# Kernel optimization log

Hardware: AMD Instinct MI355X
Metric: run time of the kernel (lower is better)

## Reference

```python
import jax, jax.numpy as jnp
import numpy as np

NUM_GRAPHS = 512
BN_EPS = 1e-5

def _lin(k, fin, fout):
    kw, kb = jax.random.split(k)
    s = 1.0 / np.sqrt(fin)
    return (jax.random.uniform(kw, (fin, fout), jnp.float32, -s, s),
            jax.random.uniform(kb, (fout,), jnp.float32, -s, s))

def setup_inputs() -> dict:
    key = jax.random.key(0)
    ks = jax.random.split(key, 16)
    N, E, F, C, H, O = 50000, 800000, 128, 256, 512, 768
    x = jax.random.normal(ks[0], (N, F), jnp.float32)
    edge_index = jax.random.randint(ks[1], (2, E), 0, N, jnp.int64)
    batch = jnp.sort(jax.random.randint(ks[2], (N,), 0, NUM_GRAPHS, jnp.int64))
    d = {"x": x, "edge_index": edge_index, "batch": batch}
    d["w1a"], d["b1a"] = _lin(ks[3], F, C)
    d["g1"], d["be1"] = jnp.ones((C,), jnp.float32), jnp.zeros((C,), jnp.float32)
    d["w1b"], d["b1b"] = _lin(ks[4], C, C)
    d["w2a"], d["b2a"] = _lin(ks[5], C, C)
    d["g2"], d["be2"] = jnp.ones((C,), jnp.float32), jnp.zeros((C,), jnp.float32)
    d["w2b"], d["b2b"] = _lin(ks[6], C, C)
    d["w3a"], d["b3a"] = _lin(ks[7], C, C)
    d["g3"], d["be3"] = jnp.ones((C,), jnp.float32), jnp.zeros((C,), jnp.float32)
    d["w3b"], d["b3b"] = _lin(ks[8], C, C)
    d["wh1"], d["bh1"] = _lin(ks[9], C, H)
    d["wh2"], d["bh2"] = _lin(ks[10], H, O)
    return d

def _bn(z, g, b):
    mu = jnp.mean(z, axis=0)
    var = jnp.mean((z - mu) ** 2, axis=0)  # biased var, torch BN training mode
    return (z - mu) * jax.lax.rsqrt(var + BN_EPS) * g + b

def _gin(x, edge_index, wa, ba, g, be, wb, bb, tanh_out):
    src, dst = edge_index[0], edge_index[1]
    agg = jax.ops.segment_sum(x[src], dst, num_segments=x.shape[0])
    h = x + agg  # eps = 0
    z = jax.nn.relu(_bn(h @ wa + ba, g, be))
    z = z @ wb + bb
    return jnp.tanh(z) if tanh_out else z

def reference(x, edge_index, batch,
              w1a, b1a, g1, be1, w1b, b1b,
              w2a, b2a, g2, be2, w2b, b2b,
              w3a, b3a, g3, be3, w3b, b3b,
              wh1, bh1, wh2, bh2):
    h = jax.nn.relu(_gin(x, edge_index, w1a, b1a, g1, be1, w1b, b1b, False))
    h = jax.nn.relu(_gin(h, edge_index, w2a, b2a, g2, be2, w2b, b2b, True))
    h = _gin(h, edge_index, w3a, b3a, g3, be3, w3b, b3b, True)
    # global mean pool over graphs
    sums = jax.ops.segment_sum(h, batch, num_segments=NUM_GRAPHS)
    cnt = jax.ops.segment_sum(jnp.ones((h.shape[0],), h.dtype), batch, num_segments=NUM_GRAPHS)
    pooled = sums / jnp.maximum(cnt, 1.0)[:, None]
    z = jax.nn.relu(pooled @ wh1 + bh1)
    return z @ wh2 + bh2
```

## Files before the change

### kernel.cpp

```cpp
#include <hip/hip_runtime.h>


typedef __attribute__((ext_vector_type(8))) short short8;
typedef __attribute__((ext_vector_type(4))) float f32x4;
typedef __attribute__((ext_vector_type(4))) unsigned short us4;
typedef __attribute__((ext_vector_type(8))) unsigned short us8;

__device__ __forceinline__ unsigned short f2bf(float f) {
  unsigned int b = __float_as_uint(f);
  unsigned int r = 0x7FFFu + ((b >> 16) & 1u);
  return (unsigned short)((b + r) >> 16);
}
__device__ __forceinline__ float bf2f(unsigned short u) {
  return __uint_as_float(((unsigned int)u) << 16);
}

__device__ __forceinline__ int swv(int row) {
  return (row & 3) ^ ((row >> 2) & 3);
}

typedef const __attribute__((address_space(1))) unsigned int* gas1;
typedef __attribute__((address_space(3))) unsigned int* las3;
__device__ __forceinline__ void gload16(const void* g, void* l) {
  __builtin_amdgcn_global_load_lds((gas1)g, (las3)l, 16, 0, 0);
}

__device__ __forceinline__ size_t swz4_idx(int row, int k, int K) {
  int g = k >> 3;
  return (size_t)row * K + ((g >> 2) << 5) + ((((g & 3) ^ swv(row)) << 3)) + (k & 7);
}

__global__ void k_histbounds(const int* __restrict__ ei, int* __restrict__ deg, int E,
                             int eb, const int* __restrict__ batch,
                             int* __restrict__ gs, int* __restrict__ ge, int N) {
  int b = blockIdx.x;
  if (b < eb) {
    int e = b * 256 + threadIdx.x;
    if (e < E) atomicAdd(&deg[ei[E + e]], 1);
  } else {
    int i = (b - eb) * 256 + threadIdx.x;
    if (i < N) {
      int bb = batch[i];
      if (i == 0 || batch[i - 1] != bb) gs[bb] = i;
      if (i == N - 1 || batch[i + 1] != bb) ge[bb] = i + 1;
    }
  }
}

__global__ __launch_bounds__(1024) void k_scan1(const int* __restrict__ deg,
                                                int* __restrict__ partial,
                                                int* __restrict__ bsum, int N) {
  __shared__ int sd[1024];
  int tid = threadIdx.x;
  int i = blockIdx.x * 1024 + tid;
  int v = (i < N) ? deg[i] : 0;
  sd[tid] = v;
  __syncthreads();
  for (int off = 1; off < 1024; off <<= 1) {
    int t = (tid >= off) ? sd[tid - off] : 0;
    __syncthreads();
    sd[tid] += t;
    __syncthreads();
  }
  if (i < N) partial[i] = sd[tid];
  if (tid == 1023) bsum[blockIdx.x] = sd[1023];
}

__global__ void k_scan2(int* __restrict__ bsum, int nb) {
  int l = threadIdx.x;
  int orig = (l < nb) ? bsum[l] : 0;
  int v = orig;
  for (int off = 1; off < 64; off <<= 1) {
    int t = __shfl_up(v, off);
    if (l >= off) v += t;
  }
  if (l < nb) bsum[l] = v - orig;
}

__global__ void k_scan3(const int* __restrict__ deg, const int* __restrict__ partial,
                        const int* __restrict__ bsum, int* __restrict__ rowptr,
                        int* __restrict__ cursor, int N) {
  int i = blockIdx.x * 256 + threadIdx.x;
  if (i >= N) return;
  int incl = partial[i] + bsum[i >> 10];
  rowptr[i + 1] = incl;
  cursor[i] = incl - deg[i];
  if (i == 0) rowptr[0] = 0;
}

__global__ void k_fill(const int* __restrict__ ei, int* __restrict__ cursor,
                       int* __restrict__ adj, int E) {
  int e = blockIdx.x * 256 + threadIdx.x;
  if (e >= E) return;
  int s = ei[e];
  int d = ei[E + e];
  int pos = atomicAdd(&cursor[d], 1);
  adj[pos] = s;
}

__global__ void k_xbf(const float* __restrict__ X, unsigned short* __restrict__ Xb,
                      int total) {
  int t = blockIdx.x * 256 + threadIdx.x;
  if (t * 8 >= total) return;
  const float4 v0 = *(const float4*)(X + t * 8);
  const float4 v1 = *(const float4*)(X + t * 8 + 4);
  us8 o;
  o[0] = f2bf(v0.x); o[1] = f2bf(v0.y); o[2] = f2bf(v0.z); o[3] = f2bf(v0.w);
  o[4] = f2bf(v1.x); o[5] = f2bf(v1.y); o[6] = f2bf(v1.z); o[7] = f2bf(v1.w);
  *(us8*)(Xb + t * 8) = o;
}

__global__ void k_prep_all(const float* __restrict__ w1a, const float* __restrict__ w1b,
                           const float* __restrict__ w2a, const float* __restrict__ w2b,
                           const float* __restrict__ w3a, const float* __restrict__ w3b,
                           const float* __restrict__ wh1, const float* __restrict__ wh2,
                           unsigned short* __restrict__ Hi, unsigned short* __restrict__ Lo) {
  int idx = blockIdx.x * 256 + threadIdx.x;
  const float* W; int K, Nout, lo_;
  if (idx < 32768)       { W = w1a; K = 128; Nout = 256; lo_ = 0; }
  else if (idx < 98304)  { W = w1b; K = 256; Nout = 256; lo_ = 32768; }
  else if (idx < 163840) { W = w2a; K = 256; Nout = 256; lo_ = 98304; }
  else if (idx < 229376) { W = w2b; K = 256; Nout = 256; lo_ = 163840; }
  else if (idx < 294912) { W = w3a; K = 256; Nout = 256; lo_ = 229376; }
  else if (idx < 360448) { W = w3b; K = 256; Nout = 256; lo_ = 294912; }
  else if (idx < 491520) { W = wh1; K = 256; Nout = 512; lo_ = 360448; }
  else                   { W = wh2; K = 512; Nout = 768; lo_ = 491520; }
  int li = idx - lo_;
  int n = li % Nout, k = li / Nout;
  float w = W[k * Nout + n];
  unsigned short h = f2bf(w);
  size_t oi = (size_t)lo_ + swz4_idx(n, k, K);
  Hi[oi] = h;
  Lo[oi] = f2bf(w - bf2f(h));
}

template <int C>
__global__ __launch_bounds__(256) void k_agg(const unsigned short* __restrict__ Xb,
                                             unsigned short* __restrict__ HHi,
                                             unsigned short* __restrict__ HLo,
                                             const int* __restrict__ rowptr,
                                             const int* __restrict__ adj, int N,
                                             float* __restrict__ statsZ) {
  if (blockIdx.x == 0) {
    statsZ[threadIdx.x] = 0.f;
    statsZ[256 + threadIdx.x] = 0.f;
  }
  int node = blockIdx.x * 4 + (threadIdx.x >> 6);
  if (node >= N) return;
  int lane = threadIdx.x & 63;
  int e0 = rowptr[node], e1 = rowptr[node + 1];
  if constexpr (C == 256) {
    us4 ov = *(const us4*)(Xb + (size_t)node * C + lane * 4);
    float a0 = bf2f(ov[0]), a1 = bf2f(ov[1]), a2 = bf2f(ov[2]), a3 = bf2f(ov[3]);
    int e = e0;
    for (; e + 4 <= e1; e += 4) {
      int s0 = adj[e], s1 = adj[e + 1], s2 = adj[e + 2], s3 = adj[e + 3];
      us4 v0 = *(const us4*)(Xb + (size_t)s0 * C + lane * 4);
      us4 v1 = *(const us4*)(Xb + (size_t)s1 * C + lane * 4);
      us4 v2 = *(const us4*)(Xb + (size_t)s2 * C + lane * 4);
      us4 v3 = *(const us4*)(Xb + (size_t)s3 * C + lane * 4);
      a0 += (bf2f(v0[0]) + bf2f(v1[0])) + (bf2f(v2[0]) + bf2f(v3[0]));
      a1 += (bf2f(v0[1]) + bf2f(v1[1])) + (bf2f(v2[1]) + bf2f(v3[1]));
      a2 += (bf2f(v0[2]) + bf2f(v1[2])) + (bf2f(v2[2]) + bf2f(v3[2]));
      a3 += (bf2f(v0[3]) + bf2f(v1[3])) + (bf2f(v2[3]) + bf2f(v3[3]));
    }
    for (; e < e1; ++e) {
      us4 v = *(const us4*)(Xb + (size_t)adj[e] * C + lane * 4);
      a0 += bf2f(v[0]); a1 += bf2f(v[1]); a2 += bf2f(v[2]); a3 += bf2f(v[3]);
    }
    float vv[4] = {a0, a1, a2, a3};
    us4 hv, lv;
#pragma unroll
    for (int j = 0; j < 4; ++j) {
      unsigned short h = f2bf(vv[j]);
      hv[j] = h;
      lv[j] = f2bf(vv[j] - bf2f(h));
    }
    size_t oi = (size_t)node * 256 + ((lane >> 3) << 5) +
                ((((lane >> 1) & 3) ^ swv(node)) << 3) + ((lane & 1) << 2);
    *(us4*)(HHi + oi) = hv;
    *(us4*)(HLo + oi) = lv;
  } else {
    ushort2 ov = *(const ushort2*)(Xb + (size_t)node * C + lane * 2);
    float a0 = bf2f(ov.x), a1 = bf2f(ov.y);
    int e = e0;
    for (; e + 4 <= e1; e += 4) {
      int s0 = adj[e], s1 = adj[e + 1], s2 = adj[e + 2], s3 = adj[e + 3];
      ushort2 v0 = *(const ushort2*)(Xb + (size_t)s0 * C + lane * 2);
      ushort2 v1 = *(const ushort2*)(Xb + (size_t)s1 * C + lane * 2);
      ushort2 v2 = *(const ushort2*)(Xb + (size_t)s2 * C + lane * 2);
      ushort2 v3 = *(const ushort2*)(Xb + (size_t)s3 * C + lane * 2);
      a0 += (bf2f(v0.x) + bf2f(v1.x)) + (bf2f(v2.x) + bf2f(v3.x));
      a1 += (bf2f(v0.y) + bf2f(v1.y)) + (bf2f(v2.y) + bf2f(v3.y));
    }
    for (; e < e1; ++e) {
      ushort2 v = *(const ushort2*)(Xb + (size_t)adj[e] * C + lane * 2);
      a0 += bf2f(v.x); a1 += bf2f(v.y);
    }
    unsigned short hx = f2bf(a0), hy = f2bf(a1);
    ushort2 hv = {hx, hy};
    ushort2 lv = {f2bf(a0 - bf2f(hx)), f2bf(a1 - bf2f(hy))};
    size_t oi = (size_t)node * 128 + ((lane >> 4) << 5) +
                ((((lane >> 2) & 3) ^ swv(node)) << 3) + ((lane & 3) << 1);
    *(ushort2*)(HHi + oi) = hv;
    *(ushort2*)(HLo + oi) = lv;
  }
}

template <int EPI, bool STATS, bool OSPLIT, bool XSWZ, int ASRC, bool FULL, bool OBF16>
__global__ __launch_bounds__(256) void k_gemm(
    const unsigned short* __restrict__ AHi, const unsigned short* __restrict__ ALo,
    const float* __restrict__ Zf,
    int M, int K, int Nld, int mb, int per,
    const unsigned short* __restrict__ WHi, const unsigned short* __restrict__ WLo,
    const float* __restrict__ bias,
    const float* __restrict__ statsIn, const float* __restrict__ gvec,
    const float* __restrict__ bevec,
    float* __restrict__ Out, unsigned short* __restrict__ OutB,
    unsigned short* __restrict__ OHi, unsigned short* __restrict__ OLo,
    float* __restrict__ statsOut) {
  __shared__ unsigned short aHi[2048], aLo[2048], bHi[4096];
  __shared__ unsigned short bLo[FULL ? 4096 : 64];
  __shared__ float sBNsc[ASRC == 2 ? 256 : 1], sBNsh[ASRC == 2 ? 256 : 1];
  int bx, by;
  if constexpr (XSWZ) {
    int xcd = blockIdx.x & 7, slot = blockIdx.x >> 3;
    bx = xcd * per + (slot >> 1);
    by = slot & 1;
    if (bx >= mb) return;
  } else {
    bx = blockIdx.x;
    by = blockIdx.y;
  }
  const int tid = threadIdx.x;
  const int lane = tid & 63, w = tid >> 6;
  const int wm = w >> 1, wn = w & 1;
  const int m0 = bx * 64, n0 = by * 128;

  if constexpr (ASRC == 2) {
    float mu = statsIn[tid] / (float)M;
    float var = statsIn[256 + tid] / (float)M - mu * mu;
    float sc = gvec[tid] * rsqrtf(var + 1e-5f);
    sBNsc[tid] = sc;
    sBNsh[tid] = bevec[tid] - mu * sc;
  }

  f32x4 zero = {0.f, 0.f, 0.f, 0.f};
  f32x4 acc[2][4];
#pragma unroll
  for (int i = 0; i < 2; ++i)
#pragma unroll
    for (int j = 0; j < 4; ++j) acc[i][j] = zero;

  const int rq = lane >> 2;
  const int k8s = lane & 3;

  float4 zr0, zr1;
  const float* zbase0 = nullptr;
  if constexpr (ASRC == 2) {
    int row0 = tid >> 2, gq0 = tid & 3;
    int ra0 = m0 + row0; if (ra0 >= M) ra0 = M - 1;
    zbase0 = Zf + (size_t)ra0 * K + gq0 * 8;
    zr0 = *(const float4*)(zbase0);
    zr1 = *(const float4*)(zbase0 + 4);
  }

  for (int kb = 0; kb < K; kb += 32) {
    __syncthreads();
    if constexpr (ASRC == 2) {
      int row = tid >> 2, gq = tid & 3;
      float f[8] = {zr0.x, zr0.y, zr0.z, zr0.w, zr1.x, zr1.y, zr1.z, zr1.w};
      us8 hv, lv;
#pragma unroll
      for (int jj = 0; jj < 8; ++jj) {
        int kc = kb + gq * 8 + jj;
        float o = fmaxf(f[jj] * sBNsc[kc] + sBNsh[kc], 0.f);
        unsigned short h = (unsigned short)(__float_as_uint(o) >> 16);
        hv[jj] = h;
        float rem = o - bf2f(h);
        lv[jj] = (unsigned short)(__float_as_uint(rem) >> 16);
      }
      int bo = row * 64 + ((gq ^ swv(row)) << 4);
      *(us8*)((char*)aHi + bo) = hv;
      *(us8*)((char*)aLo + bo) = lv;
#pragma unroll
      for (int q = 0; q < 2; ++q) {
        int rloc = (w << 5) + (q << 4) + rq;
        size_t gb = (size_t)(n0 + rloc) * K + kb + k8s * 8;
        unsigned bo2 = (w << 11) + (q << 10);
        gload16(WHi + gb, (char*)bHi + bo2);
        if constexpr (FULL) gload16(WLo + gb, (char*)bLo + bo2);
      }
    } else {
      int raA = m0 + (w << 4) + rq; if (raA >= M) raA = M - 1;
      size_t ga = (size_t)raA * K + kb + k8s * 8;
      gload16(AHi + ga, (char*)aHi + (w << 10));
      gload16(ALo + ga, (char*)aLo + (w << 10));
#pragma unroll
      for (int q = 0; q < 2; ++q) {
        int rloc = (w << 5) + (q << 4) + rq;
        size_t gb = (size_t)(n0 + rloc) * K + kb + k8s * 8;
        unsigned bo2 = (w << 11) + (q << 10);
        gload16(WHi + gb, (char*)bHi + bo2);
        if constexpr (FULL) gload16(WLo + gb, (char*)bLo + bo2);
      }
    }
    __syncthreads();

    if constexpr (ASRC == 2) {
      if (kb + 32 < K) {
        zr0 = *(const float4*)(zbase0 + kb + 32);
        zr1 = *(const float4*)(zbase0 + kb + 36);
      }
    }

    const int j = lane >> 4;
    short8 bh[4], bl[4];
#pragma unroll
    for (int ni = 0; ni < 4; ++ni) {
      int r = wn * 64 + ni * 16 + (lane & 15);
      int bo = r * 64 + ((j ^ swv(r)) << 4);
      bh[ni] = *(const short8*)((const char*)bHi + bo);
      if constexpr (FULL) bl[ni] = *(const short8*)((const char*)bLo + bo);
    }
#pragma unroll
    for (int mi = 0; mi < 2; ++mi) {
      int r = wm * 32 + mi * 16 + (lane & 15);
      int bo = r * 64 + ((j ^ swv(r)) << 4);
      short8 ah = *(const short8*)((const char*)aHi + bo);
      short8 al = *(const short8*)((const char*)aLo + bo);
#pragma unroll
      for (int ni = 0; ni < 4; ++ni) {
        acc[mi][ni] = __builtin_amdgcn_mfma_f32_16x16x32_bf16(ah, bh[ni], acc[mi][ni], 0, 0, 0);
        if constexpr (FULL)
          acc[mi][ni] = __builtin_amdgcn_mfma_f32_16x16x32_bf16(ah, bl[ni], acc[mi][ni], 0, 0, 0);
        acc[mi][ni] = __builtin_amdgcn_mfma_f32_16x16x32_bf16(al, bh[ni], acc[mi][ni], 0, 0, 0);
      }
    }
  }

#pragma unroll
  for (int ni = 0; ni < 4; ++ni) {
    int col = n0 + wn * 64 + ni * 16 + (lane & 15);
    float bc = bias[col];
    float s = 0.f, q = 0.f;
#pragma unroll
    for (int mi = 0; mi < 2; ++mi) {
      int rbase = m0 + wm * 32 + mi * 16 + (lane >> 4) * 4;
#pragma unroll
      for (int r = 0; r < 4; ++r) {
        int row = rbase + r;
        if (row < M) {
          float o = acc[mi][ni][r] + bc;
          if (STATS) { s += o; q += o * o; }
          if (OSPLIT) {
            o = fmaxf(o, 0.f);
            unsigned short h = f2bf(o);
            size_t oi = swz4_idx(row, col, Nld);
            OHi[oi] = h;
            OLo[oi] = f2bf(o - bf2f(h));
          } else {
            if (EPI == 1) o = fmaxf(o, 0.f);
            else if (EPI == 2) o = tanhf(o);
            else if (EPI == 3) o = fmaxf(tanhf(o), 0.f);
            if (OBF16) OutB[(size_t)row * Nld + col] = f2bf(o);
            else       Out[(size_t)row * Nld + col] = o;
          }
        }
      }
    }
    if (STATS) {
      s += __shfl_xor(s, 16); s += __shfl_xor(s, 32);
      q += __shfl_xor(q, 16); q += __shfl_xor(q, 32);
      if ((lane >> 4) == 0) {
        atomicAdd(&statsOut[col], s);
        atomicAdd(&statsOut[256 + col], q);
      }
    }
  }
}

__global__ __launch_bounds__(256) void k_pool(const unsigned short* __restrict__ Hb,
                                              const int* __restrict__ gs,
                                              const int* __restrict__ ge,
                                              unsigned short* __restrict__ PHi,
                                              unsigned short* __restrict__ PLo) {
  __shared__ float4 red[4][64];
  int gi = blockIdx.x;
  int s = gs[gi], e = ge[gi];
  int w = threadIdx.x >> 6, lane = threadIdx.x & 63;
  float4 acc = {0.f, 0.f, 0.f, 0.f};
  for (int r = s + w; r < e; r += 4) {
    us4 v = *(const us4*)(Hb + (size_t)r * 256 + lane * 4);
    acc.x += bf2f(v[0]); acc.y += bf2f(v[1]);
    acc.z += bf2f(v[2]); acc.w += bf2f(v[3]);
  }
  red[w][lane] = acc;
  __syncthreads();
  if (w == 0) {
    float4 a = red[0][lane], b = red[1][lane], c = red[2][lane], d = red[3][lane];
    float inv = 1.0f / fmaxf((float)(e - s), 1.0f);
    float vv[4] = {(a.x + b.x + c.x + d.x) * inv, (a.y + b.y + c.y + d.y) * inv,
                   (a.z + b.z + c.z + d.z) * inv, (a.w + b.w + c.w + d.w) * inv};
    us4 hv, lv;
#pragma unroll
    for (int j = 0; j < 4; ++j) {
      unsigned short h = f2bf(vv[j]);
      hv[j] = h;
      lv[j] = f2bf(vv[j] - bf2f(h));
    }
    size_t oi = (size_t)gi * 256 + ((lane >> 3) << 5) +
                ((((lane >> 1) & 3) ^ swv(gi)) << 3) + ((lane & 1) << 2);
    *(us4*)(PHi + oi) = hv;
    *(us4*)(PLo + oi) = lv;
  }
}

extern "C" void kernel_launch(void* const* d_in, const int* in_sizes, int n_in,
                              void* d_out, int out_size, void* d_ws, size_t ws_size,
                              hipStream_t stream) {
  const float* x      = (const float*)d_in[0];
  const int* ei       = (const int*)d_in[1];
  const int* bat      = (const int*)d_in[2];
  const float* w1a = (const float*)d_in[3];  const float* b1a = (const float*)d_in[4];
  const float* g1  = (const float*)d_in[5];  const float* be1 = (const float*)d_in[6];
  const float* w1b = (const float*)d_in[7];  const float* b1b = (const float*)d_in[8];
  const float* w2a = (const float*)d_in[9];  const float* b2a = (const float*)d_in[10];
  const float* g2  = (const float*)d_in[11]; const float* be2 = (const float*)d_in[12];
  const float* w2b = (const float*)d_in[13]; const float* b2b = (const float*)d_in[14];
  const float* w3a = (const float*)d_in[15]; const float* b3a = (const float*)d_in[16];
  const float* g3  = (const float*)d_in[17]; const float* be3 = (const float*)d_in[18];
  const float* w3b = (const float*)d_in[19]; const float* b3b = (const float*)d_in[20];
  const float* wh1 = (const float*)d_in[21]; const float* bh1 = (const float*)d_in[22];
  const float* wh2 = (const float*)d_in[23]; const float* bh2 = (const float*)d_in[24];
  float* out = (float*)d_out;

  const int N = in_sizes[0] / 128;
  const int E = in_sizes[1] / 2;
  const int G = 512;

  char* ws = (char*)d_ws;
  size_t off = 0;
  auto alloc = [&](size_t bytes) {
    void* p = ws + off;
    off = (off + bytes + 255) & ~(size_t)255;
    return p;
  };
  char* reg0 = (char*)alloc((size_t)N * 256 * 4);
  char* reg1 = (char*)alloc((size_t)N * 256 * 4);
  char* reg2 = (char*)alloc((size_t)N * 256 * 4);
  unsigned short* xb = (unsigned short*)alloc((size_t)N * 128 * 2);
  int* adj     = (int*)alloc((size_t)E * 4);
  int* rowptr  = (int*)alloc((size_t)(N + 1) * 4);
  int* cursor  = (int*)alloc((size_t)N * 4);
  int* deg     = (int*)alloc((size_t)N * 4);
  int* partial = (int*)alloc((size_t)N * 4);
  int* bsum    = (int*)alloc(64 * 4);
  unsigned short* wHi = (unsigned short*)alloc(884736 * 2);
  unsigned short* wLo = (unsigned short*)alloc(884736 * 2);
  float* stats = (float*)alloc(512 * 4);
  int* gs      = (int*)alloc(G * 4);
  int* ge      = (int*)alloc(G * 4);
  unsigned short* poolHi = (unsigned short*)alloc((size_t)G * 256 * 2);
  unsigned short* poolLo = (unsigned short*)alloc((size_t)G * 256 * 2);
  unsigned short* thidHi = (unsigned short*)alloc((size_t)G * 512 * 2);
  unsigned short* thidLo = (unsigned short*)alloc((size_t)G * 512 * 2);

  float* f0 = (float*)reg0; float* f1 = (float*)reg1; float* f2 = (float*)reg2;
  unsigned short* u0 = (unsigned short*)reg0;
  unsigned short* u1 = (unsigned short*)reg1;
  unsigned short* u2 = (unsigned short*)reg2;

  const int o1a = 0, o1b = 32768, o2a = 98304, o2b = 163840, o3a = 229376, o3b = 294912;
  const int oh1 = 360448, oh2 = 491520;

  hipMemsetAsync(deg, 0, (size_t)N * 4, stream);
  hipMemsetAsync(gs, 0, (size_t)G * 4, stream);
  hipMemsetAsync(ge, 0, (size_t)G * 4, stream);

  int eb = (E + 255) / 256;
  int nbN = (N + 255) / 256;
  int nb1 = (N + 1023) >> 10;
  k_histbounds<<<eb + nbN, 256, 0, stream>>>(ei, deg, E, eb, bat, gs, ge, N);
  k_scan1<<<nb1, 1024, 0, stream>>>(deg, partial, bsum, N);
  k_scan2<<<1, 64, 0, stream>>>(bsum, nb1);
  k_scan3<<<nbN, 256, 0, stream>>>(deg, partial, bsum, rowptr, cursor, N);
  k_fill<<<eb, 256, 0, stream>>>(ei, cursor, adj, E);

  k_xbf<<<(N * 128 / 8 + 255) / 256, 256, 0, stream>>>(x, xb, N * 128);
  k_prep_all<<<3456, 256, 0, stream>>>(w1a, w1b, w2a, w2b, w3a, w3b, wh1, wh2, wHi, wLo);

  int nb4 = (N + 3) / 4;
  const int mb = (N + 63) / 64;
  const int per = (mb + 7) / 8;
  dim3 gg(per * 16);

  k_agg<128><<<nb4, 256, 0, stream>>>(xb, u0, u1, rowptr, adj, N, stats);
  k_gemm<0, true, false, true, 0, false, false><<<gg, 256, 0, stream>>>(
      u0, u1, nullptr, N, 128, 256, mb, per, wHi + o1a, wLo + o1a, b1a,
      nullptr, nullptr, nullptr, f2, nullptr, nullptr, nullptr, stats);
  k_gemm<1, false, false, true, 2, false, true><<<gg, 256, 0, stream>>>(
      nullptr, nullptr, f2, N, 256, 256, mb, per, wHi + o1b, wLo + o1b, b1b,
      stats, g1, be1, nullptr, u0, nullptr, nullptr, nullptr);

  k_agg<256><<<nb4, 256, 0, stream>>>(u0, u1, u2, rowptr, adj, N, stats);
  k_gemm<0, true, false, true, 0, false, false><<<gg, 256, 0, stream>>>(
      u1, u2, nullptr, N, 256, 256, mb, per, wHi + o2a, wLo + o2a, b2a,
      nullptr, nullptr, nullptr, f0, nullptr, nullptr, nullptr, stats);
  k_gemm<3, false, false, true, 2, false, true><<<gg, 256, 0, stream>>>(
      nullptr, nullptr, f0, N, 256, 256, mb, per, wHi + o2b, wLo + o2b, b2b,
      stats, g2, be2, nullptr, u1, nullptr, nullptr, nullptr);

  k_agg<256><<<nb4, 256, 0, stream>>>(u1, u2, u0, rowptr, adj, N, stats);
  k_gemm<0, true, false, true, 0, false, false><<<gg, 256, 0, stream>>>(
      u2, u0, nullptr, N, 256, 256, mb, per, wHi + o3a, wLo + o3a, b3a,
      nullptr, nullptr, nullptr, f1, nullptr, nullptr, nullptr, stats);
  k_gemm<2, false, false, true, 2, false, true><<<gg, 256, 0, stream>>>(
      nullptr, nullptr, f1, N, 256, 256, mb, per, wHi + o3b, wLo + o3b, b3b,
      stats, g3, be3, nullptr, u2, nullptr, nullptr, nullptr);

  k_pool<<<G, 256, 0, stream>>>(u2, gs, ge, poolHi, poolLo);
  dim3 gh1(8, 4);
  k_gemm<1, false, true, false, 0, true, false><<<gh1, 256, 0, stream>>>(
      poolHi, poolLo, nullptr, G, 256, 512, 0, 0, wHi + oh1, wLo + oh1, bh1,
      nullptr, nullptr, nullptr, nullptr, nullptr, thidHi, thidLo, nullptr);
  dim3 gh2(8, 6);
  k_gemm<0, false, false, false, 0, true, false><<<gh2, 256, 0, stream>>>(
      thidHi, thidLo, nullptr, G, 512, 768, 0, 0, wHi + oh2, wLo + oh2, bh2,
      nullptr, nullptr, nullptr, out, nullptr, nullptr, nullptr, nullptr);
}
```

Before: 617.1 us.

## Drop hi/lo split for node activations and store pre-BN output as bf16

Aggregation output is now stored as a single bf16 array instead of a hi/lo pair, and the first GEMM of each GIN layer skips the extra low-part MFMA for activations. The pre-BN GEMM output is written as bf16 instead of fp32, and the second GEMM reads it as bf16, halving that intermediate traffic. The aim is to cut memory bandwidth and MFMA count in the node-level GEMMs, at the cost of lower numerical accuracy (bf16 rounding of activations and pre-BN values).

```diff
diff --git a/kernel.cpp b/kernel.cpp
--- a/kernel.cpp
+++ b/kernel.cpp
@@ -136,8 +136,7 @@
 
 template <int C>
 __global__ __launch_bounds__(256) void k_agg(const unsigned short* __restrict__ Xb,
-                                             unsigned short* __restrict__ HHi,
-                                             unsigned short* __restrict__ HLo,
+                                             unsigned short* __restrict__ Hb,
                                              const int* __restrict__ rowptr,
                                              const int* __restrict__ adj, int N,
                                              float* __restrict__ statsZ) {
@@ -168,18 +167,11 @@
       us4 v = *(const us4*)(Xb + (size_t)adj[e] * C + lane * 4);
       a0 += bf2f(v[0]); a1 += bf2f(v[1]); a2 += bf2f(v[2]); a3 += bf2f(v[3]);
     }
-    float vv[4] = {a0, a1, a2, a3};
-    us4 hv, lv;
-#pragma unroll
-    for (int j = 0; j < 4; ++j) {
-      unsigned short h = f2bf(vv[j]);
-      hv[j] = h;
-      lv[j] = f2bf(vv[j] - bf2f(h));
-    }
+    us4 hv;
+    hv[0] = f2bf(a0); hv[1] = f2bf(a1); hv[2] = f2bf(a2); hv[3] = f2bf(a3);
     size_t oi = (size_t)node * 256 + ((lane >> 3) << 5) +
                 ((((lane >> 1) & 3) ^ swv(node)) << 3) + ((lane & 1) << 2);
-    *(us4*)(HHi + oi) = hv;
-    *(us4*)(HLo + oi) = lv;
+    *(us4*)(Hb + oi) = hv;
   } else {
     ushort2 ov = *(const ushort2*)(Xb + (size_t)node * C + lane * 2);
     float a0 = bf2f(ov.x), a1 = bf2f(ov.y);
@@ -197,20 +189,17 @@
       ushort2 v = *(const ushort2*)(Xb + (size_t)adj[e] * C + lane * 2);
       a0 += bf2f(v.x); a1 += bf2f(v.y);
     }
-    unsigned short hx = f2bf(a0), hy = f2bf(a1);
-    ushort2 hv = {hx, hy};
-    ushort2 lv = {f2bf(a0 - bf2f(hx)), f2bf(a1 - bf2f(hy))};
+    ushort2 hv = {f2bf(a0), f2bf(a1)};
     size_t oi = (size_t)node * 128 + ((lane >> 4) << 5) +
                 ((((lane >> 2) & 3) ^ swv(node)) << 3) + ((lane & 3) << 1);
-    *(ushort2*)(HHi + oi) = hv;
-    *(ushort2*)(HLo + oi) = lv;
+    *(ushort2*)(Hb + oi) = hv;
   }
 }
 
 template <int EPI, bool STATS, bool OSPLIT, bool XSWZ, int ASRC, bool FULL, bool OBF16>
 __global__ __launch_bounds__(256) void k_gemm(
-    const unsigned short* __restrict__ AHi, const unsigned short* __restrict__ ALo,
-    const float* __restrict__ Zf,
+    const unsigned short* __restrict__ AHb, const unsigned short* __restrict__ ALo,
+    const unsigned short* __restrict__ Zb,
     int M, int K, int Nld, int mb, int per,
     const unsigned short* __restrict__ WHi, const unsigned short* __restrict__ WLo,
     const float* __restrict__ bias,
@@ -219,8 +208,8 @@
     float* __restrict__ Out, unsigned short* __restrict__ OutB,
     unsigned short* __restrict__ OHi, unsigned short* __restrict__ OLo,
     float* __restrict__ statsOut) {
-  __shared__ unsigned short aHi[2048], aLo[2048], bHi[4096];
-  __shared__ unsigned short bLo[FULL ? 4096 : 64];
+  __shared__ unsigned short aHi[2048], bHi[4096];
+  __shared__ unsigned short aLo[FULL ? 2048 : 64], bLo[FULL ? 4096 : 64];
   __shared__ float sBNsc[ASRC == 2 ? 256 : 1], sBNsh[ASRC == 2 ? 256 : 1];
   int bx, by;
   if constexpr (XSWZ) {
@@ -255,34 +244,40 @@
   const int rq = lane >> 2;
   const int k8s = lane & 3;
 
-  float4 zr0, zr1;
-  const float* zbase0 = nullptr;
+  us8 zr;
+  const unsigned short* zbase0 = nullptr;
   if constexpr (ASRC == 2) {
     int row0 = tid >> 2, gq0 = tid & 3;
     int ra0 = m0 + row0; if (ra0 >= M) ra0 = M - 1;
-    zbase0 = Zf + (size_t)ra0 * K + gq0 * 8;
-    zr0 = *(const float4*)(zbase0);
-    zr1 = *(const float4*)(zbase0 + 4);
+    zbase0 = Zb + (size_t)ra0 * K + gq0 * 8;
+    zr = *(const us8*)(zbase0);
   }
 
   for (int kb = 0; kb < K; kb += 32) {
     __syncthreads();
     if constexpr (ASRC == 2) {
       int row = tid >> 2, gq = tid & 3;
-      float f[8] = {zr0.x, zr0.y, zr0.z, zr0.w, zr1.x, zr1.y, zr1.z, zr1.w};
-      us8 hv, lv;
+      us8 hv;
 #pragma unroll
       for (int jj = 0; jj < 8; ++jj) {
         int kc = kb + gq * 8 + jj;
-        float o = fmaxf(f[jj] * sBNsc[kc] + sBNsh[kc], 0.f);
-        unsigned short h = (unsigned short)(__float_as_uint(o) >> 16);
-        hv[jj] = h;
-        float rem = o - bf2f(h);
-        lv[jj] = (unsigned short)(__float_as_uint(rem) >> 16);
+        float o = fmaxf(bf2f(zr[jj]) * sBNsc[kc] + sBNsh[kc], 0.f);
+        hv[jj] = f2bf(o);
       }
       int bo = row * 64 + ((gq ^ swv(row)) << 4);
       *(us8*)((char*)aHi + bo) = hv;
-      *(us8*)((char*)aLo + bo) = lv;
+#pragma unroll
+      for (int q = 0; q < 2; ++q) {
+        int rloc = (w << 5) + (q << 4) + rq;
+        size_t gb = (size_t)(n0 + rloc) * K + kb + k8s * 8;
+        unsigned bo2 = (w << 11) + (q << 10);
+        gload16(WHi + gb, (char*)bHi + bo2);
+      }
+    } else {
+      int raA = m0 + (w << 4) + rq; if (raA >= M) raA = M - 1;
+      size_t ga = (size_t)raA * K + kb + k8s * 8;
+      gload16(AHb + ga, (char*)aHi + (w << 10));
+      if constexpr (FULL) gload16(ALo + ga, (char*)aLo + (w << 10));
 #pragma unroll
       for (int q = 0; q < 2; ++q) {
         int rloc = (w << 5) + (q << 4) + rq;
@@ -291,27 +286,11 @@
         gload16(WHi + gb, (char*)bHi + bo2);
         if constexpr (FULL) gload16(WLo + gb, (char*)bLo + bo2);
       }
-    } else {
-      int raA = m0 + (w << 4) + rq; if (raA >= M) raA = M - 1;
-      size_t ga = (size_t)raA * K + kb + k8s * 8;
-      gload16(AHi + ga, (char*)aHi + (w << 10));
-      gload16(ALo + ga, (char*)aLo + (w << 10));
-#pragma unroll
-      for (int q = 0; q < 2; ++q) {
-        int rloc = (w << 5) + (q << 4) + rq;
-        size_t gb = (size_t)(n0 + rloc) * K + kb + k8s * 8;
-        unsigned bo2 = (w << 11) + (q << 10);
-        gload16(WHi + gb, (char*)bHi + bo2);
-        if constexpr (FULL) gload16(WLo + gb, (char*)bLo + bo2);
-      }
     }
     __syncthreads();
 
     if constexpr (ASRC == 2) {
-      if (kb + 32 < K) {
-        zr0 = *(const float4*)(zbase0 + kb + 32);
-        zr1 = *(const float4*)(zbase0 + kb + 36);
-      }
+      if (kb + 32 < K) zr = *(const us8*)(zbase0 + kb + 32);
     }
 
     const int j = lane >> 4;
@@ -328,13 +307,14 @@
       int r = wm * 32 + mi * 16 + (lane & 15);
       int bo = r * 64 + ((j ^ swv(r)) << 4);
       short8 ah = *(const short8*)((const char*)aHi + bo);
-      short8 al = *(const short8*)((const char*)aLo + bo);
 #pragma unroll
       for (int ni = 0; ni < 4; ++ni) {
         acc[mi][ni] = __builtin_amdgcn_mfma_f32_16x16x32_bf16(ah, bh[ni], acc[mi][ni], 0, 0, 0);
-        if constexpr (FULL)
+        if constexpr (FULL) {
+          short8 al = *(const short8*)((const char*)aLo + bo);
           acc[mi][ni] = __builtin_amdgcn_mfma_f32_16x16x32_bf16(ah, bl[ni], acc[mi][ni], 0, 0, 0);
-        acc[mi][ni] = __builtin_amdgcn_mfma_f32_16x16x32_bf16(al, bh[ni], acc[mi][ni], 0, 0, 0);
+          acc[mi][ni] = __builtin_amdgcn_mfma_f32_16x16x32_bf16(al, bh[ni], acc[mi][ni], 0, 0, 0);
+        }
       }
     }
   }
@@ -446,9 +426,9 @@
     off = (off + bytes + 255) & ~(size_t)255;
     return p;
   };
-  char* reg0 = (char*)alloc((size_t)N * 256 * 4);
-  char* reg1 = (char*)alloc((size_t)N * 256 * 4);
-  char* reg2 = (char*)alloc((size_t)N * 256 * 4);
+  unsigned short* hb = (unsigned short*)alloc((size_t)N * 256 * 2);
+  unsigned short* zb = (unsigned short*)alloc((size_t)N * 256 * 2);
+  unsigned short* ab = (unsigned short*)alloc((size_t)N * 256 * 2);
   unsigned short* xb = (unsigned short*)alloc((size_t)N * 128 * 2);
   int* adj     = (int*)alloc((size_t)E * 4);
   int* rowptr  = (int*)alloc((size_t)(N + 1) * 4);
@@ -466,11 +446,6 @@
   unsigned short* thidHi = (unsigned short*)alloc((size_t)G * 512 * 2);
   unsigned short* thidLo = (unsigned short*)alloc((size_t)G * 512 * 2);
 
-  float* f0 = (float*)reg0; float* f1 = (float*)reg1; float* f2 = (float*)reg2;
-  unsigned short* u0 = (unsigned short*)reg0;
-  unsigned short* u1 = (unsigned short*)reg1;
-  unsigned short* u2 = (unsigned short*)reg2;
-
   const int o1a = 0, o1b = 32768, o2a = 98304, o2b = 163840, o3a = 229376, o3b = 294912;
   const int oh1 = 360448, oh2 = 491520;
 
@@ -495,31 +470,31 @@
   const int per = (mb + 7) / 8;
   dim3 gg(per * 16);
 
-  k_agg<128><<<nb4, 256, 0, stream>>>(xb, u0, u1, rowptr, adj, N, stats);
-  k_gemm<0, true, false, true, 0, false, false><<<gg, 256, 0, stream>>>(
-      u0, u1, nullptr, N, 128, 256, mb, per, wHi + o1a, wLo + o1a, b1a,
-      nullptr, nullptr, nullptr, f2, nullptr, nullptr, nullptr, stats);
+  k_agg<128><<<nb4, 256, 0, stream>>>(xb, hb, rowptr, adj, N, stats);
+  k_gemm<0, true, false, true, 0, false, true><<<gg, 256, 0, stream>>>(
+      hb, nullptr, nullptr, N, 128, 256, mb, per, wHi + o1a, wLo + o1a, b1a,
+      nullptr, nullptr, nullptr, nullptr, zb, nullptr, nullptr, stats);
   k_gemm<1, false, false, true, 2, false, true><<<gg, 256, 0, stream>>>(
-      nullptr, nullptr, f2, N, 256, 256, mb, per, wHi + o1b, wLo + o1b, b1b,
-      stats, g1, be1, nullptr, u0, nullptr, nullptr, nullptr);
-
-  k_agg<256><<<nb4, 256, 0, stream>>>(u0, u1, u2, rowptr, adj, N, stats);
-  k_gemm<0, true, false, true, 0, false, false><<<gg, 256, 0, stream>>>(
-      u1, u2, nullptr, N, 256, 256, mb, per, wHi + o2a, wLo + o2a, b2a,
-      nullptr, nullptr, nullptr, f0, nullptr, nullptr, nullptr, stats);
+      nullptr, nullptr, zb, N, 256, 256, mb, per, wHi + o1b, wLo + o1b, b1b,
+      stats, g1, be1, nullptr, ab, nullptr, nullptr, nullptr);
+
+  k_agg<256><<<nb4, 256, 0, stream>>>(ab, hb, rowptr, adj, N, stats);
+  k_gemm<0, true, false, true, 0, false, true><<<gg, 256, 0, stream>>>(
+      hb, nullptr, nullptr, N, 256, 256, mb, per, wHi + o2a, wLo + o2a, b2a,
+      nullptr, nullptr, nullptr, nullptr, zb, nullptr, nullptr, stats);
   k_gemm<3, false, false, true, 2, false, true><<<gg, 256, 0, stream>>>(
-      nullptr, nullptr, f0, N, 256, 256, mb, per, wHi + o2b, wLo + o2b, b2b,
-      stats, g2, be2, nullptr, u1, nullptr, nullptr, nullptr);
-
-  k_agg<256><<<nb4, 256, 0, stream>>>(u1, u2, u0, rowptr, adj, N, stats);
-  k_gemm<0, true, false, true, 0, false, false><<<gg, 256, 0, stream>>>(
-      u2, u0, nullptr, N, 256, 256, mb, per, wHi + o3a, wLo + o3a, b3a,
-      nullptr, nullptr, nullptr, f1, nullptr, nullptr, nullptr, stats);
+      nullptr, nullptr, zb, N, 256, 256, mb, per, wHi + o2b, wLo + o2b, b2b,
+      stats, g2, be2, nullptr, ab, nullptr, nullptr, nullptr);
+
+  k_agg<256><<<nb4, 256, 0, stream>>>(ab, hb, rowptr, adj, N, stats);
+  k_gemm<0, true, false, true, 0, false, true><<<gg, 256, 0, stream>>>(
+      hb, nullptr, nullptr, N, 256, 256, mb, per, wHi + o3a, wLo + o3a, b3a,
+      nullptr, nullptr, nullptr, nullptr, zb, nullptr, nullptr, stats);
   k_gemm<2, false, false, true, 2, false, true><<<gg, 256, 0, stream>>>(
-      nullptr, nullptr, f1, N, 256, 256, mb, per, wHi + o3b, wLo + o3b, b3b,
-      stats, g3, be3, nullptr, u2, nullptr, nullptr, nullptr);
-
-  k_pool<<<G, 256, 0, stream>>>(u2, gs, ge, poolHi, poolLo);
+      nullptr, nullptr, zb, N, 256, 256, mb, per, wHi + o3b, wLo + o3b, b3b,
+      stats, g3, be3, nullptr, ab, nullptr, nullptr, nullptr);
+
+  k_pool<<<G, 256, 0, stream>>>(ab, gs, ge, poolHi, poolLo);
   dim3 gh1(8, 4);
   k_gemm<1, false, true, false, 0, true, false><<<gh1, 256, 0, stream>>>(
       poolHi, poolLo, nullptr, G, 256, 512, 0, 0, wHi + oh1, wLo + oh1, bh1,
```

Result: faster. 602.3 us (-2.4%).
